# Kernel optimization log

Hardware: AMD Instinct MI355X
Metric: run time of the kernel (lower is better)

The kernel has to match this reference:

```python
import jax, jax.numpy as jnp
import numpy as np

F = 256

def setup_inputs() -> dict:
    key = jax.random.key(0)
    ks = jax.random.split(key, 6)
    s = 1.0 / np.sqrt(F)
    x = jax.random.normal(ks[0], (16, 1024, F), dtype=jnp.float32)
    W_alpha = jax.random.uniform(ks[1], (F, F), minval=-s, maxval=s, dtype=jnp.float32)
    W_beta = jax.random.uniform(ks[2], (F, F), minval=-s, maxval=s, dtype=jnp.float32)
    W_unary = jax.random.uniform(ks[3], (F, F), minval=-s, maxval=s, dtype=jnp.float32)
    b_unary = jax.random.uniform(ks[4], (F,), minval=-s, maxval=s, dtype=jnp.float32)
    W_r = jax.random.uniform(ks[5], (F, F), minval=-s, maxval=s, dtype=jnp.float32)
    return {"x": x, "W_alpha": W_alpha, "W_beta": W_beta, "W_unary": W_unary, "b_unary": b_unary, "W_r": W_r}

def reference(x, W_alpha, W_beta, W_unary, b_unary, W_r):
    # x: [B, N, F]; torch Linear computes x @ W^T (+ b)
    B, N, _ = x.shape
    alpha = jnp.einsum('bnf,gf->bng', x, W_alpha)
    beta = jnp.einsum('bnf,gf->bng', x, W_beta)
    unary = jnp.einsum('bnf,gf->bng', x, W_unary) + b_unary
    # scores: alpha_i . beta_j, diagonal excluded (i == j skipped in loop)
    scores = jnp.einsum('bif,bjf->bij', alpha, beta)
    scores = scores * (1.0 - jnp.eye(N, dtype=x.dtype))
    att = jnp.einsum('bij,bjf->bif', scores, unary) / N
    out = jnp.einsum('bif,gf->big', att, W_r) + x
    return out
```

## Files before the change

kernel.cpp:

```cpp
#include <hip/hip_runtime.h>


typedef __bf16 bf16;
typedef float floatx4 __attribute__((ext_vector_type(4)));
typedef bf16 bf16x8 __attribute__((ext_vector_type(8)));
typedef bf16 bf16x4 __attribute__((ext_vector_type(4)));

constexpr int FD = 256;
constexpr int NB = 16;
constexpr int NN = 1024;
constexpr int RR = NB * NN;

__device__ __forceinline__ bf16x8 cvt8(float4 a, float4 b) {
    bf16x8 o = { (bf16)a.x, (bf16)a.y, (bf16)a.z, (bf16)a.w,
                 (bf16)b.x, (bf16)b.y, (bf16)b.z, (bf16)b.w };
    return o;
}

__global__ __launch_bounds__(256)
void prep(const float* __restrict__ Wu, const float* __restrict__ bu, const float* __restrict__ Wr,
          bf16* __restrict__ Wcb, float* __restrict__ bc)
{
    const int blk = blockIdx.x, tid = threadIdx.x;
    if (blk < 256) {
        const int j = blk;
        float acc = 0.0f;
        for (int g = 0; g < FD; g += 4) {
            float4 wr = *(const float4*)&Wr[j * FD + g];
            acc += wr.x * Wu[g * FD + tid] + wr.y * Wu[(g + 1) * FD + tid]
                 + wr.z * Wu[(g + 2) * FD + tid] + wr.w * Wu[(g + 3) * FD + tid];
        }
        Wcb[j * FD + tid] = (bf16)acc;
    } else {
        float s = 0.0f;
        for (int g = 0; g < FD; g++) s += Wr[tid * FD + g] * bu[g];
        bc[tid] = s;
    }
}

__global__ __launch_bounds__(256)
void proj3(const float* __restrict__ x,
           const float* __restrict__ Wa, const float* __restrict__ Wb, const bf16* __restrict__ Wc,
           bf16* __restrict__ alpha, bf16* __restrict__ U2,
           bf16* __restrict__ betaT, bf16* __restrict__ U2T,
           const float* __restrict__ bc, float* __restrict__ dpart)
{
    constexpr int BM = 128, BN = 64, BK = 32, LDK = 36;
    __shared__ bf16 As[BM][LDK];
    __shared__ bf16 Bs[3][BN][LDK];
    __shared__ bf16 Tr[8960];
    const int tid = threadIdx.x;
    const int wave = tid >> 6, lane = tid & 63;
    const int q = lane >> 4, l16 = lane & 15;
    const int bm = blockIdx.y * BM, bn = blockIdx.x * BN;

    const int rowA0 = tid >> 2,          k8A0 = (tid & 3) * 8;
    const int rowA1 = (tid + 256) >> 2,  k8A1 = (tid & 3) * 8;
    const int rowW  = tid >> 2,          k8W  = (tid & 3) * 8;

    bf16x8 pxa0, pxa1, pwa, pwb; int4 pwc;
#define PROJ_LOAD(KK) do { \
        const float* s0 = &x[(size_t)(bm + rowA0) * FD + (KK) + k8A0]; \
        pxa0 = cvt8(*(const float4*)s0, *(const float4*)(s0 + 4)); \
        const float* s1 = &x[(size_t)(bm + rowA1) * FD + (KK) + k8A1]; \
        pxa1 = cvt8(*(const float4*)s1, *(const float4*)(s1 + 4)); \
        const float* sa = &Wa[(size_t)(bn + rowW) * FD + (KK) + k8W]; \
        pwa = cvt8(*(const float4*)sa, *(const float4*)(sa + 4)); \
        const float* sb = &Wb[(size_t)(bn + rowW) * FD + (KK) + k8W]; \
        pwb = cvt8(*(const float4*)sb, *(const float4*)(sb + 4)); \
        pwc = *(const int4*)&Wc[(size_t)(bn + rowW) * FD + (KK) + k8W]; \
    } while (0)

    floatx4 acc[3][2][4] = {};
    PROJ_LOAD(0);

    for (int k0 = 0; k0 < FD; k0 += BK) {
        *(bf16x8*)&As[rowA0][k8A0] = pxa0;
        *(bf16x8*)&As[rowA1][k8A1] = pxa1;
        *(bf16x8*)&Bs[0][rowW][k8W] = pwa;
        *(bf16x8*)&Bs[1][rowW][k8W] = pwb;
        *(int4*)&Bs[2][rowW][k8W] = pwc;
        __syncthreads();
        if (k0 + BK < FD) PROJ_LOAD(k0 + BK);
        bf16x8 af[2];
        #pragma unroll
        for (int mi = 0; mi < 2; mi++)
            af[mi] = *(const bf16x8*)&As[wave * 32 + mi * 16 + l16][q * 8];
        #pragma unroll
        for (int w = 0; w < 3; w++) {
            bf16x8 bq[4];
            #pragma unroll
            for (int nj = 0; nj < 4; nj++)
                bq[nj] = *(const bf16x8*)&Bs[w][nj * 16 + l16][q * 8];
            #pragma unroll
            for (int mi = 0; mi < 2; mi++)
                #pragma unroll
                for (int nj = 0; nj < 4; nj++)
                    acc[w][mi][nj] = __builtin_amdgcn_mfma_f32_16x16x32_bf16(af[mi], bq[nj], acc[w][mi][nj], 0, 0, 0);
        }
        __syncthreads();
    }
#undef PROJ_LOAD

    const int b = bm >> 10, n0 = bm & (NN - 1);
    float bcv[4];
    #pragma unroll
    for (int nj = 0; nj < 4; nj++) bcv[nj] = bc[bn + nj * 16 + l16];

    #pragma unroll
    for (int mi = 0; mi < 2; mi++)
        #pragma unroll
        for (int i = 0; i < 4; i++) {
            float p = 0.0f;
            #pragma unroll
            for (int nj = 0; nj < 4; nj++)
                p += acc[0][mi][nj][i] * acc[1][mi][nj][i];
            #pragma unroll
            for (int off = 1; off < 16; off <<= 1) p += __shfl_xor(p, off);
            if (l16 == 0) {
                int m = bm + wave * 32 + mi * 16 + q * 4 + i;
                dpart[(size_t)blockIdx.x * RR + m] = p;
            }
        }

    #pragma unroll
    for (int pass = 0; pass < 2; pass++) {
        const int w = pass ? 2 : 0;
        __syncthreads();
        #pragma unroll
        for (int mi = 0; mi < 2; mi++)
            #pragma unroll
            for (int i = 0; i < 4; i++) {
                int ml = wave * 32 + mi * 16 + q * 4 + i;
                #pragma unroll
                for (int nj = 0; nj < 4; nj++) {
                    float v = acc[w][mi][nj][i];
                    if (w == 2) v += bcv[nj];
                    Tr[ml * 68 + nj * 16 + l16] = (bf16)v;
                }
            }
        __syncthreads();
        bf16* dst = pass ? U2 : alpha;
        #pragma unroll
        for (int it = 0; it < 4; it++) {
            int c = tid + it * 256;
            int row = c >> 3, chunk = c & 7;
            bf16x8 v = *(const bf16x8*)&Tr[row * 68 + chunk * 8];
            *(bf16x8*)&dst[(size_t)(bm + row) * FD + bn + chunk * 8] = v;
        }
    }

    #pragma unroll
    for (int pass = 0; pass < 2; pass++) {
        const int w = pass ? 2 : 1;
        __syncthreads();
        #pragma unroll
        for (int mi = 0; mi < 2; mi++)
            #pragma unroll
            for (int nj = 0; nj < 4; nj++) {
                bf16x4 v4;
                #pragma unroll
                for (int i = 0; i < 4; i++) {
                    float v = acc[w][mi][nj][i];
                    if (w == 2) v += bcv[nj];
                    v4[i] = (bf16)v;
                }
                *(bf16x4*)&Tr[(nj * 16 + l16) * 140 + wave * 32 + mi * 16 + q * 4] = v4;
            }
        __syncthreads();
        bf16* dst = (pass ? U2T : betaT) + (size_t)b * FD * NN;
        #pragma unroll
        for (int it = 0; it < 4; it++) {
            int c = tid + it * 256;
            int row = c >> 4, chunk = c & 15;
            bf16x8 v = *(const bf16x8*)&Tr[row * 140 + chunk * 8];
            *(bf16x8*)&dst[(size_t)(bn + row) * NN + n0 + chunk * 8] = v;
        }
    }
}

__global__ __launch_bounds__(256)
void m2_mfma(const bf16* __restrict__ U2T, const bf16* __restrict__ betaT, bf16* __restrict__ M2t)
{
    constexpr int LDK = 36;
    __shared__ bf16 As[64][LDK];
    __shared__ bf16 Bs[64][LDK];
    __shared__ bf16 Tr[64 * 68];
    const int tid = threadIdx.x;
    const int wave = tid >> 6, lane = tid & 63;
    const int q = lane >> 4, l16 = lane & 15;
    const int wj = wave >> 1, wk = wave & 1;
    const int b = blockIdx.z;
    const int bj = blockIdx.y * 64, bk = blockIdx.x * 64;
    const int row = tid >> 2, k8 = (tid & 3) * 8;
    const bf16* Arow = U2T + (size_t)b * FD * NN + (size_t)(bj + row) * NN + k8;
    const bf16* Brow = betaT + (size_t)b * FD * NN + (size_t)(bk + row) * NN + k8;

    int4 ra = *(const int4*)&Arow[0];
    int4 rb = *(const int4*)&Brow[0];
    floatx4 acc[2][2] = {};
    for (int n0 = 0; n0 < NN; n0 += 32) {
        *(int4*)&As[row][k8] = ra;
        *(int4*)&Bs[row][k8] = rb;
        __syncthreads();
        if (n0 + 32 < NN) { ra = *(const int4*)&Arow[n0 + 32]; rb = *(const int4*)&Brow[n0 + 32]; }
        bf16x8 af[2], bq[2];
        #pragma unroll
        for (int mi = 0; mi < 2; mi++)
            af[mi] = *(const bf16x8*)&As[wj * 32 + mi * 16 + l16][q * 8];
        #pragma unroll
        for (int kj = 0; kj < 2; kj++)
            bq[kj] = *(const bf16x8*)&Bs[wk * 32 + kj * 16 + l16][q * 8];
        #pragma unroll
        for (int mi = 0; mi < 2; mi++)
            #pragma unroll
            for (int kj = 0; kj < 2; kj++)
                acc[mi][kj] = __builtin_amdgcn_mfma_f32_16x16x32_bf16(af[mi], bq[kj], acc[mi][kj], 0, 0, 0);
        __syncthreads();
    }
    __syncthreads();
    #pragma unroll
    for (int mi = 0; mi < 2; mi++)
        #pragma unroll
        for (int i = 0; i < 4; i++) {
            int jl = wj * 32 + mi * 16 + q * 4 + i;
            #pragma unroll
            for (int kj = 0; kj < 2; kj++)
                Tr[jl * 68 + wk * 32 + kj * 16 + l16] = (bf16)acc[mi][kj][i];
        }
    __syncthreads();
    bf16* Mb = M2t + (size_t)b * FD * FD;
    #pragma unroll
    for (int it = 0; it < 2; it++) {
        int c = tid + it * 256;
        int r = c >> 3, chunk = c & 7;
        bf16x8 v = *(const bf16x8*)&Tr[r * 68 + chunk * 8];
        *(bf16x8*)&Mb[(size_t)(bj + r) * FD + bk + chunk * 8] = v;
    }
}

__global__ __launch_bounds__(256)
void final_mfma(const bf16* __restrict__ alpha, const bf16* __restrict__ M2t,
                const float* __restrict__ dpart, const bf16* __restrict__ U2,
                const float* __restrict__ x, float* __restrict__ out)
{
    constexpr int BM = 128, BN = 64, BK = 32, LDK = 36;
    __shared__ bf16 As[BM][LDK];
    __shared__ bf16 Bs[BN][LDK];
    const int tid = threadIdx.x;
    const int wave = tid >> 6, lane = tid & 63;
    const int q = lane >> 4, l16 = lane & 15;
    const int bm = blockIdx.y * BM, bn = blockIdx.x * BN;
    const bf16* Qb = M2t + (size_t)(bm >> 10) * FD * FD;

    const int rowA0 = tid >> 2,         k8A0 = (tid & 3) * 8;
    const int rowA1 = (tid + 256) >> 2, k8A1 = (tid & 3) * 8;
    const int rowB  = tid >> 2,         k8B  = (tid & 3) * 8;

    int4 ra0 = *(const int4*)&alpha[(size_t)(bm + rowA0) * FD + k8A0];
    int4 ra1 = *(const int4*)&alpha[(size_t)(bm + rowA1) * FD + k8A1];
    int4 rb  = *(const int4*)&Qb[(size_t)(bn + rowB) * FD + k8B];

    floatx4 acc[2][4] = {};
    for (int k0 = 0; k0 < FD; k0 += BK) {
        *(int4*)&As[rowA0][k8A0] = ra0;
        *(int4*)&As[rowA1][k8A1] = ra1;
        *(int4*)&Bs[rowB][k8B] = rb;
        __syncthreads();
        if (k0 + BK < FD) {
            ra0 = *(const int4*)&alpha[(size_t)(bm + rowA0) * FD + k0 + BK + k8A0];
            ra1 = *(const int4*)&alpha[(size_t)(bm + rowA1) * FD + k0 + BK + k8A1];
            rb  = *(const int4*)&Qb[(size_t)(bn + rowB) * FD + k0 + BK + k8B];
        }
        bf16x8 af[2], bq[4];
        #pragma unroll
        for (int mi = 0; mi < 2; mi++)
            af[mi] = *(const bf16x8*)&As[wave * 32 + mi * 16 + l16][q * 8];
        #pragma unroll
        for (int nj = 0; nj < 4; nj++)
            bq[nj] = *(const bf16x8*)&Bs[nj * 16 + l16][q * 8];
        #pragma unroll
        for (int mi = 0; mi < 2; mi++)
            #pragma unroll
            for (int nj = 0; nj < 4; nj++)
                acc[mi][nj] = __builtin_amdgcn_mfma_f32_16x16x32_bf16(af[mi], bq[nj], acc[mi][nj], 0, 0, 0);
        __syncthreads();
    }

    #pragma unroll
    for (int mi = 0; mi < 2; mi++)
        #pragma unroll
        for (int i = 0; i < 4; i++) {
            int m = bm + wave * 32 + mi * 16 + q * 4 + i;
            float d = dpart[m] + dpart[RR + m] + dpart[2 * RR + m] + dpart[3 * RR + m];
            #pragma unroll
            for (int nj = 0; nj < 4; nj++) {
                int n = bn + nj * 16 + l16;
                float v = (acc[mi][nj][i] - d * (float)U2[(size_t)m * FD + n]) * (1.0f / 1024.0f);
                out[(size_t)m * FD + n] = v + x[(size_t)m * FD + n];
            }
        }
}

extern "C" void kernel_launch(void* const* d_in, const int* in_sizes, int n_in,
                              void* d_out, int out_size, void* d_ws, size_t ws_size,
                              hipStream_t stream)
{
    const float* x  = (const float*)d_in[0];
    const float* Wa = (const float*)d_in[1];
    const float* Wb = (const float*)d_in[2];
    const float* Wu = (const float*)d_in[3];
    const float* bu = (const float*)d_in[4];
    const float* Wr = (const float*)d_in[5];
    float* out = (float*)d_out;

    char* w = (char*)d_ws;
    bf16* Wcb   = (bf16*)w;  w += (size_t)FD * FD * 2;
    float* bc   = (float*)w; w += (size_t)FD * 4;
    bf16* alpha = (bf16*)w;  w += (size_t)RR * FD * 2;
    bf16* U2    = (bf16*)w;  w += (size_t)RR * FD * 2;
    bf16* betaT = (bf16*)w;  w += (size_t)RR * FD * 2;
    bf16* U2T   = (bf16*)w;  w += (size_t)RR * FD * 2;
    bf16* M2t   = (bf16*)w;  w += (size_t)NB * FD * FD * 2;
    float* dpart= (float*)w; w += (size_t)4 * RR * 4;

    dim3 blk(256);

    prep<<<dim3(257), blk, 0, stream>>>(Wu, bu, Wr, Wcb, bc);

    proj3<<<dim3(FD / 64, RR / 128), blk, 0, stream>>>(x, Wa, Wb, Wcb,
                                                       alpha, U2, betaT, U2T, bc, dpart);

    m2_mfma<<<dim3(FD / 64, FD / 64, NB), blk, 0, stream>>>(U2T, betaT, M2t);

    final_mfma<<<dim3(FD / 64, RR / 128), blk, 0, stream>>>(alpha, M2t, dpart, U2, x, out);
}
```

Baseline: 127.8 us.

## Split-K the M2 reduction, shrink proj/final tiles to 64x64 with BK=64

The M2 GEMM over the sequence dimension is split into four chunks across more blocks, writing fp32 partials that a new reduction kernel sums and converts to bf16. The proj3 and final kernels move from 128-row to 64-row tiles with a K-step of 64 and a wider LDS row stride, which doubles their grid size. The goal is more parallelism and occupancy, since m2 previously launched only 256 blocks. The cost is an extra kernel launch, fp32 partial traffic, and more redundant weight loads per row tile.

```diff
diff --git a/kernel.cpp b/kernel.cpp
--- a/kernel.cpp
+++ b/kernel.cpp
@@ -45,58 +45,64 @@
            bf16* __restrict__ betaT, bf16* __restrict__ U2T,
            const float* __restrict__ bc, float* __restrict__ dpart)
 {
-    constexpr int BM = 128, BN = 64, BK = 32, LDK = 36;
-    __shared__ bf16 As[BM][LDK];
-    __shared__ bf16 Bs[3][BN][LDK];
-    __shared__ bf16 Tr[8960];
+    constexpr int LDK = 68, WSZ = 64 * LDK;
+    __shared__ __align__(16) bf16 smem[4 * WSZ];
+    bf16* As = smem;
+    bf16* Bs = smem + WSZ;
+    bf16* Tr = smem;
     const int tid = threadIdx.x;
     const int wave = tid >> 6, lane = tid & 63;
     const int q = lane >> 4, l16 = lane & 15;
-    const int bm = blockIdx.y * BM, bn = blockIdx.x * BN;
-
-    const int rowA0 = tid >> 2,          k8A0 = (tid & 3) * 8;
-    const int rowA1 = (tid + 256) >> 2,  k8A1 = (tid & 3) * 8;
-    const int rowW  = tid >> 2,          k8W  = (tid & 3) * 8;
-
-    bf16x8 pxa0, pxa1, pwa, pwb; int4 pwc;
+    const int bm = blockIdx.y * 64, bn = blockIdx.x * 64;
+
+    const int row0 = tid >> 3, k8 = (tid & 7) * 8;
+
+    bf16x8 pA[2], pW0[2], pW1[2]; int4 pW2[2];
 #define PROJ_LOAD(KK) do { \
-        const float* s0 = &x[(size_t)(bm + rowA0) * FD + (KK) + k8A0]; \
-        pxa0 = cvt8(*(const float4*)s0, *(const float4*)(s0 + 4)); \
-        const float* s1 = &x[(size_t)(bm + rowA1) * FD + (KK) + k8A1]; \
-        pxa1 = cvt8(*(const float4*)s1, *(const float4*)(s1 + 4)); \
-        const float* sa = &Wa[(size_t)(bn + rowW) * FD + (KK) + k8W]; \
-        pwa = cvt8(*(const float4*)sa, *(const float4*)(sa + 4)); \
-        const float* sb = &Wb[(size_t)(bn + rowW) * FD + (KK) + k8W]; \
-        pwb = cvt8(*(const float4*)sb, *(const float4*)(sb + 4)); \
-        pwc = *(const int4*)&Wc[(size_t)(bn + rowW) * FD + (KK) + k8W]; \
+        const float* s0 = &x[(size_t)(bm + row0) * FD + (KK) + k8]; \
+        pA[0] = cvt8(*(const float4*)s0, *(const float4*)(s0 + 4)); \
+        const float* s1 = &x[(size_t)(bm + row0 + 32) * FD + (KK) + k8]; \
+        pA[1] = cvt8(*(const float4*)s1, *(const float4*)(s1 + 4)); \
+        const float* a0 = &Wa[(size_t)(bn + row0) * FD + (KK) + k8]; \
+        pW0[0] = cvt8(*(const float4*)a0, *(const float4*)(a0 + 4)); \
+        const float* a1 = &Wa[(size_t)(bn + row0 + 32) * FD + (KK) + k8]; \
+        pW0[1] = cvt8(*(const float4*)a1, *(const float4*)(a1 + 4)); \
+        const float* b0 = &Wb[(size_t)(bn + row0) * FD + (KK) + k8]; \
+        pW1[0] = cvt8(*(const float4*)b0, *(const float4*)(b0 + 4)); \
+        const float* b1 = &Wb[(size_t)(bn + row0 + 32) * FD + (KK) + k8]; \
+        pW1[1] = cvt8(*(const float4*)b1, *(const float4*)(b1 + 4)); \
+        pW2[0] = *(const int4*)&Wc[(size_t)(bn + row0) * FD + (KK) + k8]; \
+        pW2[1] = *(const int4*)&Wc[(size_t)(bn + row0 + 32) * FD + (KK) + k8]; \
     } while (0)
 
-    floatx4 acc[3][2][4] = {};
+    floatx4 acc[3][4] = {};
     PROJ_LOAD(0);
 
-    for (int k0 = 0; k0 < FD; k0 += BK) {
-        *(bf16x8*)&As[rowA0][k8A0] = pxa0;
-        *(bf16x8*)&As[rowA1][k8A1] = pxa1;
-        *(bf16x8*)&Bs[0][rowW][k8W] = pwa;
-        *(bf16x8*)&Bs[1][rowW][k8W] = pwb;
-        *(int4*)&Bs[2][rowW][k8W] = pwc;
-        __syncthreads();
-        if (k0 + BK < FD) PROJ_LOAD(k0 + BK);
+    for (int k0 = 0; k0 < FD; k0 += 64) {
+        *(bf16x8*)&As[row0 * LDK + k8] = pA[0];
+        *(bf16x8*)&As[(row0 + 32) * LDK + k8] = pA[1];
+        *(bf16x8*)&Bs[0 * WSZ + row0 * LDK + k8] = pW0[0];
+        *(bf16x8*)&Bs[0 * WSZ + (row0 + 32) * LDK + k8] = pW0[1];
+        *(bf16x8*)&Bs[1 * WSZ + row0 * LDK + k8] = pW1[0];
+        *(bf16x8*)&Bs[1 * WSZ + (row0 + 32) * LDK + k8] = pW1[1];
+        *(int4*)&Bs[2 * WSZ + row0 * LDK + k8] = pW2[0];
+        *(int4*)&Bs[2 * WSZ + (row0 + 32) * LDK + k8] = pW2[1];
+        __syncthreads();
+        if (k0 + 64 < FD) PROJ_LOAD(k0 + 64);
         bf16x8 af[2];
         #pragma unroll
-        for (int mi = 0; mi < 2; mi++)
-            af[mi] = *(const bf16x8*)&As[wave * 32 + mi * 16 + l16][q * 8];
+        for (int h = 0; h < 2; h++)
+            af[h] = *(const bf16x8*)&As[(wave * 16 + l16) * LDK + h * 32 + q * 8];
         #pragma unroll
         for (int w = 0; w < 3; w++) {
-            bf16x8 bq[4];
-            #pragma unroll
-            for (int nj = 0; nj < 4; nj++)
-                bq[nj] = *(const bf16x8*)&Bs[w][nj * 16 + l16][q * 8];
-            #pragma unroll
-            for (int mi = 0; mi < 2; mi++)
+            #pragma unroll
+            for (int h = 0; h < 2; h++) {
                 #pragma unroll
-                for (int nj = 0; nj < 4; nj++)
-                    acc[w][mi][nj] = __builtin_amdgcn_mfma_f32_16x16x32_bf16(af[mi], bq[nj], acc[w][mi][nj], 0, 0, 0);
+                for (int nj = 0; nj < 4; nj++) {
+                    bf16x8 bq = *(const bf16x8*)&Bs[w * WSZ + (nj * 16 + l16) * LDK + h * 32 + q * 8];
+                    acc[w][nj] = __builtin_amdgcn_mfma_f32_16x16x32_bf16(af[h], bq, acc[w][nj], 0, 0, 0);
+                }
+            }
         }
         __syncthreads();
     }
@@ -108,41 +114,37 @@
     for (int nj = 0; nj < 4; nj++) bcv[nj] = bc[bn + nj * 16 + l16];
 
     #pragma unroll
-    for (int mi = 0; mi < 2; mi++)
-        #pragma unroll
-        for (int i = 0; i < 4; i++) {
-            float p = 0.0f;
-            #pragma unroll
-            for (int nj = 0; nj < 4; nj++)
-                p += acc[0][mi][nj][i] * acc[1][mi][nj][i];
-            #pragma unroll
-            for (int off = 1; off < 16; off <<= 1) p += __shfl_xor(p, off);
-            if (l16 == 0) {
-                int m = bm + wave * 32 + mi * 16 + q * 4 + i;
-                dpart[(size_t)blockIdx.x * RR + m] = p;
-            }
-        }
+    for (int i = 0; i < 4; i++) {
+        float p = 0.0f;
+        #pragma unroll
+        for (int nj = 0; nj < 4; nj++)
+            p += acc[0][nj][i] * acc[1][nj][i];
+        #pragma unroll
+        for (int off = 1; off < 16; off <<= 1) p += __shfl_xor(p, off);
+        if (l16 == 0) {
+            int m = bm + wave * 16 + q * 4 + i;
+            dpart[(size_t)blockIdx.x * RR + m] = p;
+        }
+    }
 
     #pragma unroll
     for (int pass = 0; pass < 2; pass++) {
         const int w = pass ? 2 : 0;
         __syncthreads();
         #pragma unroll
-        for (int mi = 0; mi < 2; mi++)
-            #pragma unroll
-            for (int i = 0; i < 4; i++) {
-                int ml = wave * 32 + mi * 16 + q * 4 + i;
-                #pragma unroll
-                for (int nj = 0; nj < 4; nj++) {
-                    float v = acc[w][mi][nj][i];
-                    if (w == 2) v += bcv[nj];
-                    Tr[ml * 68 + nj * 16 + l16] = (bf16)v;
-                }
+        for (int i = 0; i < 4; i++) {
+            int ml = wave * 16 + q * 4 + i;
+            #pragma unroll
+            for (int nj = 0; nj < 4; nj++) {
+                float v = acc[w][nj][i];
+                if (w == 2) v += bcv[nj];
+                Tr[ml * 68 + nj * 16 + l16] = (bf16)v;
             }
+        }
         __syncthreads();
         bf16* dst = pass ? U2 : alpha;
         #pragma unroll
-        for (int it = 0; it < 4; it++) {
+        for (int it = 0; it < 2; it++) {
             int c = tid + it * 256;
             int row = c >> 3, chunk = c & 7;
             bf16x8 v = *(const bf16x8*)&Tr[row * 68 + chunk * 8];
@@ -155,88 +157,109 @@
         const int w = pass ? 2 : 1;
         __syncthreads();
         #pragma unroll
-        for (int mi = 0; mi < 2; mi++)
-            #pragma unroll
-            for (int nj = 0; nj < 4; nj++) {
-                bf16x4 v4;
-                #pragma unroll
-                for (int i = 0; i < 4; i++) {
-                    float v = acc[w][mi][nj][i];
-                    if (w == 2) v += bcv[nj];
-                    v4[i] = (bf16)v;
-                }
-                *(bf16x4*)&Tr[(nj * 16 + l16) * 140 + wave * 32 + mi * 16 + q * 4] = v4;
+        for (int nj = 0; nj < 4; nj++) {
+            bf16x4 v4;
+            #pragma unroll
+            for (int i = 0; i < 4; i++) {
+                float v = acc[w][nj][i];
+                if (w == 2) v += bcv[nj];
+                v4[i] = (bf16)v;
             }
+            *(bf16x4*)&Tr[(nj * 16 + l16) * 72 + wave * 16 + q * 4] = v4;
+        }
         __syncthreads();
         bf16* dst = (pass ? U2T : betaT) + (size_t)b * FD * NN;
         #pragma unroll
-        for (int it = 0; it < 4; it++) {
+        for (int it = 0; it < 2; it++) {
             int c = tid + it * 256;
-            int row = c >> 4, chunk = c & 15;
-            bf16x8 v = *(const bf16x8*)&Tr[row * 140 + chunk * 8];
+            int row = c >> 3, chunk = c & 7;
+            bf16x8 v = *(const bf16x8*)&Tr[row * 72 + chunk * 8];
             *(bf16x8*)&dst[(size_t)(bn + row) * NN + n0 + chunk * 8] = v;
         }
     }
 }
 
 __global__ __launch_bounds__(256)
-void m2_mfma(const bf16* __restrict__ U2T, const bf16* __restrict__ betaT, bf16* __restrict__ M2t)
-{
-    constexpr int LDK = 36;
-    __shared__ bf16 As[64][LDK];
-    __shared__ bf16 Bs[64][LDK];
-    __shared__ bf16 Tr[64 * 68];
+void m2_mfma(const bf16* __restrict__ U2T, const bf16* __restrict__ betaT, float* __restrict__ Mpart)
+{
+    constexpr int LDK = 68;
+    __shared__ __align__(16) bf16 As[64 * LDK];
+    __shared__ __align__(16) bf16 Bs[64 * LDK];
     const int tid = threadIdx.x;
     const int wave = tid >> 6, lane = tid & 63;
     const int q = lane >> 4, l16 = lane & 15;
     const int wj = wave >> 1, wk = wave & 1;
-    const int b = blockIdx.z;
+    const int b = blockIdx.z >> 2, ch = blockIdx.z & 3;
     const int bj = blockIdx.y * 64, bk = blockIdx.x * 64;
-    const int row = tid >> 2, k8 = (tid & 3) * 8;
-    const bf16* Arow = U2T + (size_t)b * FD * NN + (size_t)(bj + row) * NN + k8;
-    const bf16* Brow = betaT + (size_t)b * FD * NN + (size_t)(bk + row) * NN + k8;
-
-    int4 ra = *(const int4*)&Arow[0];
-    int4 rb = *(const int4*)&Brow[0];
+    const int nb = ch * 256;
+    const int row0 = tid >> 3, k8 = (tid & 7) * 8;
+    const bf16* Ap = U2T + (size_t)b * FD * NN;
+    const bf16* Bp = betaT + (size_t)b * FD * NN;
+
+    int4 ra[2], rb[2];
+    ra[0] = *(const int4*)&Ap[(size_t)(bj + row0) * NN + nb + k8];
+    ra[1] = *(const int4*)&Ap[(size_t)(bj + row0 + 32) * NN + nb + k8];
+    rb[0] = *(const int4*)&Bp[(size_t)(bk + row0) * NN + nb + k8];
+    rb[1] = *(const int4*)&Bp[(size_t)(bk + row0 + 32) * NN + nb + k8];
+
     floatx4 acc[2][2] = {};
-    for (int n0 = 0; n0 < NN; n0 += 32) {
-        *(int4*)&As[row][k8] = ra;
-        *(int4*)&Bs[row][k8] = rb;
-        __syncthreads();
-        if (n0 + 32 < NN) { ra = *(const int4*)&Arow[n0 + 32]; rb = *(const int4*)&Brow[n0 + 32]; }
-        bf16x8 af[2], bq[2];
-        #pragma unroll
-        for (int mi = 0; mi < 2; mi++)
-            af[mi] = *(const bf16x8*)&As[wj * 32 + mi * 16 + l16][q * 8];
-        #pragma unroll
-        for (int kj = 0; kj < 2; kj++)
-            bq[kj] = *(const bf16x8*)&Bs[wk * 32 + kj * 16 + l16][q * 8];
-        #pragma unroll
-        for (int mi = 0; mi < 2; mi++)
+    for (int nc = 0; nc < 256; nc += 64) {
+        *(int4*)&As[row0 * LDK + k8] = ra[0];
+        *(int4*)&As[(row0 + 32) * LDK + k8] = ra[1];
+        *(int4*)&Bs[row0 * LDK + k8] = rb[0];
+        *(int4*)&Bs[(row0 + 32) * LDK + k8] = rb[1];
+        __syncthreads();
+        if (nc + 64 < 256) {
+            int nn = nb + nc + 64;
+            ra[0] = *(const int4*)&Ap[(size_t)(bj + row0) * NN + nn + k8];
+            ra[1] = *(const int4*)&Ap[(size_t)(bj + row0 + 32) * NN + nn + k8];
+            rb[0] = *(const int4*)&Bp[(size_t)(bk + row0) * NN + nn + k8];
+            rb[1] = *(const int4*)&Bp[(size_t)(bk + row0 + 32) * NN + nn + k8];
+        }
+        #pragma unroll
+        for (int h = 0; h < 2; h++) {
+            bf16x8 af[2], bq[2];
+            #pragma unroll
+            for (int mi = 0; mi < 2; mi++)
+                af[mi] = *(const bf16x8*)&As[(wj * 32 + mi * 16 + l16) * LDK + h * 32 + q * 8];
             #pragma unroll
             for (int kj = 0; kj < 2; kj++)
-                acc[mi][kj] = __builtin_amdgcn_mfma_f32_16x16x32_bf16(af[mi], bq[kj], acc[mi][kj], 0, 0, 0);
-        __syncthreads();
-    }
-    __syncthreads();
+                bq[kj] = *(const bf16x8*)&Bs[(wk * 32 + kj * 16 + l16) * LDK + h * 32 + q * 8];
+            #pragma unroll
+            for (int mi = 0; mi < 2; mi++)
+                #pragma unroll
+                for (int kj = 0; kj < 2; kj++)
+                    acc[mi][kj] = __builtin_amdgcn_mfma_f32_16x16x32_bf16(af[mi], bq[kj], acc[mi][kj], 0, 0, 0);
+        }
+        __syncthreads();
+    }
+
+    float* P = Mpart + ((size_t)ch * NB + b) * FD * FD;
     #pragma unroll
     for (int mi = 0; mi < 2; mi++)
         #pragma unroll
         for (int i = 0; i < 4; i++) {
-            int jl = wj * 32 + mi * 16 + q * 4 + i;
+            int j = bj + wj * 32 + mi * 16 + q * 4 + i;
             #pragma unroll
             for (int kj = 0; kj < 2; kj++)
-                Tr[jl * 68 + wk * 32 + kj * 16 + l16] = (bf16)acc[mi][kj][i];
-        }
-    __syncthreads();
-    bf16* Mb = M2t + (size_t)b * FD * FD;
-    #pragma unroll
-    for (int it = 0; it < 2; it++) {
-        int c = tid + it * 256;
-        int r = c >> 3, chunk = c & 7;
-        bf16x8 v = *(const bf16x8*)&Tr[r * 68 + chunk * 8];
-        *(bf16x8*)&Mb[(size_t)(bj + r) * FD + bk + chunk * 8] = v;
-    }
+                P[(size_t)j * FD + bk + wk * 32 + kj * 16 + l16] = acc[mi][kj][i];
+        }
+}
+
+__global__ __launch_bounds__(256)
+void mred(const float* __restrict__ Mpart, bf16* __restrict__ M2t)
+{
+    const size_t S = (size_t)NB * FD * FD;
+    size_t i = ((size_t)blockIdx.x * 256 + threadIdx.x) * 8;
+    float4 a0 = *(const float4*)&Mpart[i],         a1 = *(const float4*)&Mpart[i + 4];
+    float4 b0 = *(const float4*)&Mpart[S + i],     b1 = *(const float4*)&Mpart[S + i + 4];
+    float4 c0 = *(const float4*)&Mpart[2*S + i],   c1 = *(const float4*)&Mpart[2*S + i + 4];
+    float4 d0 = *(const float4*)&Mpart[3*S + i],   d1 = *(const float4*)&Mpart[3*S + i + 4];
+    bf16x8 o = { (bf16)(a0.x + b0.x + c0.x + d0.x), (bf16)(a0.y + b0.y + c0.y + d0.y),
+                 (bf16)(a0.z + b0.z + c0.z + d0.z), (bf16)(a0.w + b0.w + c0.w + d0.w),
+                 (bf16)(a1.x + b1.x + c1.x + d1.x), (bf16)(a1.y + b1.y + c1.y + d1.y),
+                 (bf16)(a1.z + b1.z + c1.z + d1.z), (bf16)(a1.w + b1.w + c1.w + d1.w) };
+    *(bf16x8*)&M2t[i] = o;
 }
 
 __global__ __launch_bounds__(256)
@@ -244,62 +267,58 @@
                 const float* __restrict__ dpart, const bf16* __restrict__ U2,
                 const float* __restrict__ x, float* __restrict__ out)
 {
-    constexpr int BM = 128, BN = 64, BK = 32, LDK = 36;
-    __shared__ bf16 As[BM][LDK];
-    __shared__ bf16 Bs[BN][LDK];
+    constexpr int LDK = 68;
+    __shared__ __align__(16) bf16 As[64 * LDK];
+    __shared__ __align__(16) bf16 Bs[64 * LDK];
     const int tid = threadIdx.x;
     const int wave = tid >> 6, lane = tid & 63;
     const int q = lane >> 4, l16 = lane & 15;
-    const int bm = blockIdx.y * BM, bn = blockIdx.x * BN;
+    const int bm = blockIdx.y * 64, bn = blockIdx.x * 64;
     const bf16* Qb = M2t + (size_t)(bm >> 10) * FD * FD;
-
-    const int rowA0 = tid >> 2,         k8A0 = (tid & 3) * 8;
-    const int rowA1 = (tid + 256) >> 2, k8A1 = (tid & 3) * 8;
-    const int rowB  = tid >> 2,         k8B  = (tid & 3) * 8;
-
-    int4 ra0 = *(const int4*)&alpha[(size_t)(bm + rowA0) * FD + k8A0];
-    int4 ra1 = *(const int4*)&alpha[(size_t)(bm + rowA1) * FD + k8A1];
-    int4 rb  = *(const int4*)&Qb[(size_t)(bn + rowB) * FD + k8B];
-
-    floatx4 acc[2][4] = {};
-    for (int k0 = 0; k0 < FD; k0 += BK) {
-        *(int4*)&As[rowA0][k8A0] = ra0;
-        *(int4*)&As[rowA1][k8A1] = ra1;
-        *(int4*)&Bs[rowB][k8B] = rb;
-        __syncthreads();
-        if (k0 + BK < FD) {
-            ra0 = *(const int4*)&alpha[(size_t)(bm + rowA0) * FD + k0 + BK + k8A0];
-            ra1 = *(const int4*)&alpha[(size_t)(bm + rowA1) * FD + k0 + BK + k8A1];
-            rb  = *(const int4*)&Qb[(size_t)(bn + rowB) * FD + k0 + BK + k8B];
-        }
-        bf16x8 af[2], bq[4];
-        #pragma unroll
-        for (int mi = 0; mi < 2; mi++)
-            af[mi] = *(const bf16x8*)&As[wave * 32 + mi * 16 + l16][q * 8];
-        #pragma unroll
-        for (int nj = 0; nj < 4; nj++)
-            bq[nj] = *(const bf16x8*)&Bs[nj * 16 + l16][q * 8];
-        #pragma unroll
-        for (int mi = 0; mi < 2; mi++)
-            #pragma unroll
-            for (int nj = 0; nj < 4; nj++)
-                acc[mi][nj] = __builtin_amdgcn_mfma_f32_16x16x32_bf16(af[mi], bq[nj], acc[mi][nj], 0, 0, 0);
-        __syncthreads();
-    }
-
-    #pragma unroll
-    for (int mi = 0; mi < 2; mi++)
-        #pragma unroll
-        for (int i = 0; i < 4; i++) {
-            int m = bm + wave * 32 + mi * 16 + q * 4 + i;
-            float d = dpart[m] + dpart[RR + m] + dpart[2 * RR + m] + dpart[3 * RR + m];
+    const int row0 = tid >> 3, k8 = (tid & 7) * 8;
+
+    int4 ra[2], rb[2];
+    ra[0] = *(const int4*)&alpha[(size_t)(bm + row0) * FD + k8];
+    ra[1] = *(const int4*)&alpha[(size_t)(bm + row0 + 32) * FD + k8];
+    rb[0] = *(const int4*)&Qb[(size_t)(bn + row0) * FD + k8];
+    rb[1] = *(const int4*)&Qb[(size_t)(bn + row0 + 32) * FD + k8];
+
+    floatx4 acc[4] = {};
+    for (int k0 = 0; k0 < FD; k0 += 64) {
+        *(int4*)&As[row0 * LDK + k8] = ra[0];
+        *(int4*)&As[(row0 + 32) * LDK + k8] = ra[1];
+        *(int4*)&Bs[row0 * LDK + k8] = rb[0];
+        *(int4*)&Bs[(row0 + 32) * LDK + k8] = rb[1];
+        __syncthreads();
+        if (k0 + 64 < FD) {
+            ra[0] = *(const int4*)&alpha[(size_t)(bm + row0) * FD + k0 + 64 + k8];
+            ra[1] = *(const int4*)&alpha[(size_t)(bm + row0 + 32) * FD + k0 + 64 + k8];
+            rb[0] = *(const int4*)&Qb[(size_t)(bn + row0) * FD + k0 + 64 + k8];
+            rb[1] = *(const int4*)&Qb[(size_t)(bn + row0 + 32) * FD + k0 + 64 + k8];
+        }
+        #pragma unroll
+        for (int h = 0; h < 2; h++) {
+            bf16x8 af = *(const bf16x8*)&As[(wave * 16 + l16) * LDK + h * 32 + q * 8];
             #pragma unroll
             for (int nj = 0; nj < 4; nj++) {
-                int n = bn + nj * 16 + l16;
-                float v = (acc[mi][nj][i] - d * (float)U2[(size_t)m * FD + n]) * (1.0f / 1024.0f);
-                out[(size_t)m * FD + n] = v + x[(size_t)m * FD + n];
+                bf16x8 bq = *(const bf16x8*)&Bs[(nj * 16 + l16) * LDK + h * 32 + q * 8];
+                acc[nj] = __builtin_amdgcn_mfma_f32_16x16x32_bf16(af, bq, acc[nj], 0, 0, 0);
             }
         }
+        __syncthreads();
+    }
+
+    #pragma unroll
+    for (int i = 0; i < 4; i++) {
+        int m = bm + wave * 16 + q * 4 + i;
+        float d = dpart[m] + dpart[RR + m] + dpart[2 * RR + m] + dpart[3 * RR + m];
+        #pragma unroll
+        for (int nj = 0; nj < 4; nj++) {
+            int n = bn + nj * 16 + l16;
+            float v = (acc[nj][i] - d * (float)U2[(size_t)m * FD + n]) * (1.0f / 1024.0f);
+            out[(size_t)m * FD + n] = v + x[(size_t)m * FD + n];
+        }
+    }
 }
 
 extern "C" void kernel_launch(void* const* d_in, const int* in_sizes, int n_in,
@@ -323,15 +342,18 @@
     bf16* U2T   = (bf16*)w;  w += (size_t)RR * FD * 2;
     bf16* M2t   = (bf16*)w;  w += (size_t)NB * FD * FD * 2;
     float* dpart= (float*)w; w += (size_t)4 * RR * 4;
+    float* Mpart= (float*)w; w += (size_t)4 * NB * FD * FD * 4;
 
     dim3 blk(256);
 
     prep<<<dim3(257), blk, 0, stream>>>(Wu, bu, Wr, Wcb, bc);
 
-    proj3<<<dim3(FD / 64, RR / 128), blk, 0, stream>>>(x, Wa, Wb, Wcb,
-                                                       alpha, U2, betaT, U2T, bc, dpart);
-
-    m2_mfma<<<dim3(FD / 64, FD / 64, NB), blk, 0, stream>>>(U2T, betaT, M2t);
-
-    final_mfma<<<dim3(FD / 64, RR / 128), blk, 0, stream>>>(alpha, M2t, dpart, U2, x, out);
-}
+    proj3<<<dim3(FD / 64, RR / 64), blk, 0, stream>>>(x, Wa, Wb, Wcb,
+                                                      alpha, U2, betaT, U2T, bc, dpart);
+
+    m2_mfma<<<dim3(FD / 64, FD / 64, NB * 4), blk, 0, stream>>>(U2T, betaT, Mpart);
+
+    mred<<<dim3(512), blk, 0, stream>>>(Mpart, M2t);
+
+    final_mfma<<<dim3(FD / 64, RR / 64), blk, 0, stream>>>(alpha, M2t, dpart, U2, x, out);
+}
```

After: 202.0 us. +58.0%, slower.

## Fuse all stages into one cooperative persistent kernel with grid syncs

Applied to the files above, without the earlier changes.

Merges the prep, projection, M2 and final GEMM kernels into a single cooperative launch of 512 blocks that separates stages with grid.sync. Prep now also converts Wa and Wb to bf16 so the projection loads bf16 weights directly. The M2 stage uses a 64-wide K step to halve the number of loop iterations. The aim is to remove launch gaps and per-block conversion work. In exchange there are grid-wide barriers, a fixed grid size that limits parallelism in each stage, and a fallback to separate kernels if the cooperative launch fails.

```diff
diff --git a/kernel.cpp b/kernel.cpp
--- a/kernel.cpp
+++ b/kernel.cpp
@@ -1,4 +1,7 @@
 #include <hip/hip_runtime.h>
+#include <hip/hip_cooperative_groups.h>
+
+namespace cg = cooperative_groups;
 
 
 typedef __bf16 bf16;
@@ -17,81 +20,91 @@
     return o;
 }
 
-__global__ __launch_bounds__(256)
-void prep(const float* __restrict__ Wu, const float* __restrict__ bu, const float* __restrict__ Wr,
-          bf16* __restrict__ Wcb, float* __restrict__ bc)
-{
-    const int blk = blockIdx.x, tid = threadIdx.x;
-    if (blk < 256) {
-        const int j = blk;
-        float acc = 0.0f;
-        for (int g = 0; g < FD; g += 4) {
-            float4 wr = *(const float4*)&Wr[j * FD + g];
-            acc += wr.x * Wu[g * FD + tid] + wr.y * Wu[(g + 1) * FD + tid]
-                 + wr.z * Wu[(g + 2) * FD + tid] + wr.w * Wu[(g + 3) * FD + tid];
-        }
-        Wcb[j * FD + tid] = (bf16)acc;
-    } else {
+__device__ __forceinline__ void dev_prep(int blk, int tid,
+    const float* __restrict__ Wa, const float* __restrict__ Wb,
+    const float* __restrict__ Wu, const float* __restrict__ bu, const float* __restrict__ Wr,
+    bf16* __restrict__ Wab, bf16* __restrict__ Wbb, bf16* __restrict__ Wcb, float* __restrict__ bc)
+{
+    if (blk < 16) {
+        int w = blk >> 3, wb = blk & 7;
+        const float* src = (w == 0) ? Wa : Wb;
+        bf16* dst = (w == 0) ? Wab : Wbb;
+        for (int it = 0; it < 8; it++) {
+            int i = wb * 8192 + it * 1024 + tid * 4;
+            float4 v = *(const float4*)&src[i];
+            bf16x4 o = { (bf16)v.x, (bf16)v.y, (bf16)v.z, (bf16)v.w };
+            *(bf16x4*)&dst[i] = o;
+        }
+    } else if (blk < 80) {
+        int j0 = (blk - 16) * 4;
+        float acc[4] = {};
+        for (int g = 0; g < FD; g++) {
+            float wu = Wu[g * FD + tid];
+            #pragma unroll
+            for (int jr = 0; jr < 4; jr++)
+                acc[jr] += Wr[(j0 + jr) * FD + g] * wu;
+        }
+        #pragma unroll
+        for (int jr = 0; jr < 4; jr++)
+            Wcb[(j0 + jr) * FD + tid] = (bf16)acc[jr];
+    } else if (blk == 80) {
         float s = 0.0f;
         for (int g = 0; g < FD; g++) s += Wr[tid * FD + g] * bu[g];
         bc[tid] = s;
     }
 }
 
-__global__ __launch_bounds__(256)
-void proj3(const float* __restrict__ x,
-           const float* __restrict__ Wa, const float* __restrict__ Wb, const bf16* __restrict__ Wc,
-           bf16* __restrict__ alpha, bf16* __restrict__ U2,
-           bf16* __restrict__ betaT, bf16* __restrict__ U2T,
-           const float* __restrict__ bc, float* __restrict__ dpart)
-{
-    constexpr int BM = 128, BN = 64, BK = 32, LDK = 36;
-    __shared__ bf16 As[BM][LDK];
-    __shared__ bf16 Bs[3][BN][LDK];
-    __shared__ bf16 Tr[8960];
-    const int tid = threadIdx.x;
+__device__ __forceinline__ void dev_proj(int bx, int by, int tid, char* smemraw,
+    const float* __restrict__ x,
+    const bf16* __restrict__ Wab, const bf16* __restrict__ Wbb, const bf16* __restrict__ Wcb,
+    const float* __restrict__ bc,
+    bf16* __restrict__ alpha, bf16* __restrict__ U2,
+    bf16* __restrict__ betaT, bf16* __restrict__ U2T, float* __restrict__ dpart)
+{
+    constexpr int LDK = 36;
+    bf16* As = (bf16*)smemraw;
+    bf16* Bs = (bf16*)(smemraw + 9216);
+    bf16* Tr = (bf16*)(smemraw + 23040);
     const int wave = tid >> 6, lane = tid & 63;
     const int q = lane >> 4, l16 = lane & 15;
-    const int bm = blockIdx.y * BM, bn = blockIdx.x * BN;
-
-    const int rowA0 = tid >> 2,          k8A0 = (tid & 3) * 8;
-    const int rowA1 = (tid + 256) >> 2,  k8A1 = (tid & 3) * 8;
-    const int rowW  = tid >> 2,          k8W  = (tid & 3) * 8;
-
-    bf16x8 pxa0, pxa1, pwa, pwb; int4 pwc;
-#define PROJ_LOAD(KK) do { \
-        const float* s0 = &x[(size_t)(bm + rowA0) * FD + (KK) + k8A0]; \
+    const int bm = by * 128, bn = bx * 64;
+
+    const int rowA0 = tid >> 2, k8A = (tid & 3) * 8;
+    const int rowA1 = rowA0 + 64;
+    const int rowW = tid >> 2, k8W = (tid & 3) * 8;
+
+    bf16x8 pxa0, pxa1; int4 pwa, pwb, pwc;
+#define PLOAD(KK) do { \
+        const float* s0 = &x[(size_t)(bm + rowA0) * FD + (KK) + k8A]; \
         pxa0 = cvt8(*(const float4*)s0, *(const float4*)(s0 + 4)); \
-        const float* s1 = &x[(size_t)(bm + rowA1) * FD + (KK) + k8A1]; \
+        const float* s1 = &x[(size_t)(bm + rowA1) * FD + (KK) + k8A]; \
         pxa1 = cvt8(*(const float4*)s1, *(const float4*)(s1 + 4)); \
-        const float* sa = &Wa[(size_t)(bn + rowW) * FD + (KK) + k8W]; \
-        pwa = cvt8(*(const float4*)sa, *(const float4*)(sa + 4)); \
-        const float* sb = &Wb[(size_t)(bn + rowW) * FD + (KK) + k8W]; \
-        pwb = cvt8(*(const float4*)sb, *(const float4*)(sb + 4)); \
-        pwc = *(const int4*)&Wc[(size_t)(bn + rowW) * FD + (KK) + k8W]; \
+        pwa = *(const int4*)&Wab[(size_t)(bn + rowW) * FD + (KK) + k8W]; \
+        pwb = *(const int4*)&Wbb[(size_t)(bn + rowW) * FD + (KK) + k8W]; \
+        pwc = *(const int4*)&Wcb[(size_t)(bn + rowW) * FD + (KK) + k8W]; \
     } while (0)
 
     floatx4 acc[3][2][4] = {};
-    PROJ_LOAD(0);
-
-    for (int k0 = 0; k0 < FD; k0 += BK) {
-        *(bf16x8*)&As[rowA0][k8A0] = pxa0;
-        *(bf16x8*)&As[rowA1][k8A1] = pxa1;
-        *(bf16x8*)&Bs[0][rowW][k8W] = pwa;
-        *(bf16x8*)&Bs[1][rowW][k8W] = pwb;
-        *(int4*)&Bs[2][rowW][k8W] = pwc;
-        __syncthreads();
-        if (k0 + BK < FD) PROJ_LOAD(k0 + BK);
+    PLOAD(0);
+
+    for (int k0 = 0; k0 < FD; k0 += 32) {
+        *(bf16x8*)&As[rowA0 * LDK + k8A] = pxa0;
+        *(bf16x8*)&As[rowA1 * LDK + k8A] = pxa1;
+        *(int4*)&Bs[(0 * 64 + rowW) * LDK + k8W] = pwa;
+        *(int4*)&Bs[(1 * 64 + rowW) * LDK + k8W] = pwb;
+        *(int4*)&Bs[(2 * 64 + rowW) * LDK + k8W] = pwc;
+        __syncthreads();
+        if (k0 + 32 < FD) PLOAD(k0 + 32);
         bf16x8 af[2];
         #pragma unroll
         for (int mi = 0; mi < 2; mi++)
-            af[mi] = *(const bf16x8*)&As[wave * 32 + mi * 16 + l16][q * 8];
+            af[mi] = *(const bf16x8*)&As[(wave * 32 + mi * 16 + l16) * LDK + q * 8];
         #pragma unroll
         for (int w = 0; w < 3; w++) {
             bf16x8 bq[4];
             #pragma unroll
             for (int nj = 0; nj < 4; nj++)
-                bq[nj] = *(const bf16x8*)&Bs[w][nj * 16 + l16][q * 8];
+                bq[nj] = *(const bf16x8*)&Bs[(w * 64 + nj * 16 + l16) * LDK + q * 8];
             #pragma unroll
             for (int mi = 0; mi < 2; mi++)
                 #pragma unroll
@@ -100,7 +113,7 @@
         }
         __syncthreads();
     }
-#undef PROJ_LOAD
+#undef PLOAD
 
     const int b = bm >> 10, n0 = bm & (NN - 1);
     float bcv[4];
@@ -119,7 +132,7 @@
             for (int off = 1; off < 16; off <<= 1) p += __shfl_xor(p, off);
             if (l16 == 0) {
                 int m = bm + wave * 32 + mi * 16 + q * 4 + i;
-                dpart[(size_t)blockIdx.x * RR + m] = p;
+                dpart[(size_t)bx * RR + m] = p;
             }
         }
 
@@ -179,43 +192,56 @@
     }
 }
 
-__global__ __launch_bounds__(256)
-void m2_mfma(const bf16* __restrict__ U2T, const bf16* __restrict__ betaT, bf16* __restrict__ M2t)
-{
-    constexpr int LDK = 36;
-    __shared__ bf16 As[64][LDK];
-    __shared__ bf16 Bs[64][LDK];
-    __shared__ bf16 Tr[64 * 68];
-    const int tid = threadIdx.x;
+__device__ __forceinline__ void dev_m2(int blk, int tid, char* smemraw,
+    const bf16* __restrict__ U2T, const bf16* __restrict__ betaT, bf16* __restrict__ M2t)
+{
+    constexpr int LDK = 68;
+    bf16* As = (bf16*)smemraw;
+    bf16* Bs = (bf16*)(smemraw + 8704);
+    bf16* Tr = (bf16*)(smemraw + 17408);
     const int wave = tid >> 6, lane = tid & 63;
     const int q = lane >> 4, l16 = lane & 15;
     const int wj = wave >> 1, wk = wave & 1;
-    const int b = blockIdx.z;
-    const int bj = blockIdx.y * 64, bk = blockIdx.x * 64;
-    const int row = tid >> 2, k8 = (tid & 3) * 8;
-    const bf16* Arow = U2T + (size_t)b * FD * NN + (size_t)(bj + row) * NN + k8;
-    const bf16* Brow = betaT + (size_t)b * FD * NN + (size_t)(bk + row) * NN + k8;
-
-    int4 ra = *(const int4*)&Arow[0];
-    int4 rb = *(const int4*)&Brow[0];
+    const int b = blk >> 4, rem = blk & 15;
+    const int bj = (rem >> 2) * 64, bk = (rem & 3) * 64;
+    const int row0 = tid >> 3, k8 = (tid & 7) * 8;
+    const bf16* Ap = U2T + (size_t)b * FD * NN;
+    const bf16* Bp = betaT + (size_t)b * FD * NN;
+
+    int4 ra[2], rb[2];
+    ra[0] = *(const int4*)&Ap[(size_t)(bj + row0) * NN + k8];
+    ra[1] = *(const int4*)&Ap[(size_t)(bj + row0 + 32) * NN + k8];
+    rb[0] = *(const int4*)&Bp[(size_t)(bk + row0) * NN + k8];
+    rb[1] = *(const int4*)&Bp[(size_t)(bk + row0 + 32) * NN + k8];
+
     floatx4 acc[2][2] = {};
-    for (int n0 = 0; n0 < NN; n0 += 32) {
-        *(int4*)&As[row][k8] = ra;
-        *(int4*)&Bs[row][k8] = rb;
-        __syncthreads();
-        if (n0 + 32 < NN) { ra = *(const int4*)&Arow[n0 + 32]; rb = *(const int4*)&Brow[n0 + 32]; }
-        bf16x8 af[2], bq[2];
-        #pragma unroll
-        for (int mi = 0; mi < 2; mi++)
-            af[mi] = *(const bf16x8*)&As[wj * 32 + mi * 16 + l16][q * 8];
-        #pragma unroll
-        for (int kj = 0; kj < 2; kj++)
-            bq[kj] = *(const bf16x8*)&Bs[wk * 32 + kj * 16 + l16][q * 8];
-        #pragma unroll
-        for (int mi = 0; mi < 2; mi++)
+    for (int n0 = 0; n0 < NN; n0 += 64) {
+        *(int4*)&As[row0 * LDK + k8] = ra[0];
+        *(int4*)&As[(row0 + 32) * LDK + k8] = ra[1];
+        *(int4*)&Bs[row0 * LDK + k8] = rb[0];
+        *(int4*)&Bs[(row0 + 32) * LDK + k8] = rb[1];
+        __syncthreads();
+        if (n0 + 64 < NN) {
+            ra[0] = *(const int4*)&Ap[(size_t)(bj + row0) * NN + n0 + 64 + k8];
+            ra[1] = *(const int4*)&Ap[(size_t)(bj + row0 + 32) * NN + n0 + 64 + k8];
+            rb[0] = *(const int4*)&Bp[(size_t)(bk + row0) * NN + n0 + 64 + k8];
+            rb[1] = *(const int4*)&Bp[(size_t)(bk + row0 + 32) * NN + n0 + 64 + k8];
+        }
+        #pragma unroll
+        for (int h = 0; h < 2; h++) {
+            bf16x8 af[2], bq[2];
+            #pragma unroll
+            for (int mi = 0; mi < 2; mi++)
+                af[mi] = *(const bf16x8*)&As[(wj * 32 + mi * 16 + l16) * LDK + h * 32 + q * 8];
             #pragma unroll
             for (int kj = 0; kj < 2; kj++)
-                acc[mi][kj] = __builtin_amdgcn_mfma_f32_16x16x32_bf16(af[mi], bq[kj], acc[mi][kj], 0, 0, 0);
+                bq[kj] = *(const bf16x8*)&Bs[(wk * 32 + kj * 16 + l16) * LDK + h * 32 + q * 8];
+            #pragma unroll
+            for (int mi = 0; mi < 2; mi++)
+                #pragma unroll
+                for (int kj = 0; kj < 2; kj++)
+                    acc[mi][kj] = __builtin_amdgcn_mfma_f32_16x16x32_bf16(af[mi], bq[kj], acc[mi][kj], 0, 0, 0);
+        }
         __syncthreads();
     }
     __syncthreads();
@@ -239,46 +265,45 @@
     }
 }
 
-__global__ __launch_bounds__(256)
-void final_mfma(const bf16* __restrict__ alpha, const bf16* __restrict__ M2t,
-                const float* __restrict__ dpart, const bf16* __restrict__ U2,
-                const float* __restrict__ x, float* __restrict__ out)
-{
-    constexpr int BM = 128, BN = 64, BK = 32, LDK = 36;
-    __shared__ bf16 As[BM][LDK];
-    __shared__ bf16 Bs[BN][LDK];
-    const int tid = threadIdx.x;
+__device__ __forceinline__ void dev_final(int bx, int by, int tid, char* smemraw,
+    const bf16* __restrict__ alpha, const bf16* __restrict__ M2t,
+    const float* __restrict__ dpart, const bf16* __restrict__ U2,
+    const float* __restrict__ x, float* __restrict__ out)
+{
+    constexpr int LDK = 36;
+    bf16* As = (bf16*)smemraw;
+    bf16* Bs = (bf16*)(smemraw + 9216);
     const int wave = tid >> 6, lane = tid & 63;
     const int q = lane >> 4, l16 = lane & 15;
-    const int bm = blockIdx.y * BM, bn = blockIdx.x * BN;
+    const int bm = by * 128, bn = bx * 64;
     const bf16* Qb = M2t + (size_t)(bm >> 10) * FD * FD;
 
-    const int rowA0 = tid >> 2,         k8A0 = (tid & 3) * 8;
-    const int rowA1 = (tid + 256) >> 2, k8A1 = (tid & 3) * 8;
-    const int rowB  = tid >> 2,         k8B  = (tid & 3) * 8;
-
-    int4 ra0 = *(const int4*)&alpha[(size_t)(bm + rowA0) * FD + k8A0];
-    int4 ra1 = *(const int4*)&alpha[(size_t)(bm + rowA1) * FD + k8A1];
+    const int rowA0 = tid >> 2, k8A = (tid & 3) * 8;
+    const int rowA1 = rowA0 + 64;
+    const int rowB = tid >> 2, k8B = (tid & 3) * 8;
+
+    int4 ra0 = *(const int4*)&alpha[(size_t)(bm + rowA0) * FD + k8A];
+    int4 ra1 = *(const int4*)&alpha[(size_t)(bm + rowA1) * FD + k8A];
     int4 rb  = *(const int4*)&Qb[(size_t)(bn + rowB) * FD + k8B];
 
     floatx4 acc[2][4] = {};
-    for (int k0 = 0; k0 < FD; k0 += BK) {
-        *(int4*)&As[rowA0][k8A0] = ra0;
-        *(int4*)&As[rowA1][k8A1] = ra1;
-        *(int4*)&Bs[rowB][k8B] = rb;
-        __syncthreads();
-        if (k0 + BK < FD) {
-            ra0 = *(const int4*)&alpha[(size_t)(bm + rowA0) * FD + k0 + BK + k8A0];
-            ra1 = *(const int4*)&alpha[(size_t)(bm + rowA1) * FD + k0 + BK + k8A1];
-            rb  = *(const int4*)&Qb[(size_t)(bn + rowB) * FD + k0 + BK + k8B];
+    for (int k0 = 0; k0 < FD; k0 += 32) {
+        *(int4*)&As[rowA0 * LDK + k8A] = ra0;
+        *(int4*)&As[rowA1 * LDK + k8A] = ra1;
+        *(int4*)&Bs[rowB * LDK + k8B] = rb;
+        __syncthreads();
+        if (k0 + 32 < FD) {
+            ra0 = *(const int4*)&alpha[(size_t)(bm + rowA0) * FD + k0 + 32 + k8A];
+            ra1 = *(const int4*)&alpha[(size_t)(bm + rowA1) * FD + k0 + 32 + k8A];
+            rb  = *(const int4*)&Qb[(size_t)(bn + rowB) * FD + k0 + 32 + k8B];
         }
         bf16x8 af[2], bq[4];
         #pragma unroll
         for (int mi = 0; mi < 2; mi++)
-            af[mi] = *(const bf16x8*)&As[wave * 32 + mi * 16 + l16][q * 8];
+            af[mi] = *(const bf16x8*)&As[(wave * 32 + mi * 16 + l16) * LDK + q * 8];
         #pragma unroll
         for (int nj = 0; nj < 4; nj++)
-            bq[nj] = *(const bf16x8*)&Bs[nj * 16 + l16][q * 8];
+            bq[nj] = *(const bf16x8*)&Bs[(nj * 16 + l16) * LDK + q * 8];
         #pragma unroll
         for (int mi = 0; mi < 2; mi++)
             #pragma unroll
@@ -300,6 +325,62 @@
                 out[(size_t)m * FD + n] = v + x[(size_t)m * FD + n];
             }
         }
+}
+
+__global__ __launch_bounds__(256, 2)
+void fused(const float* x, const float* Wa, const float* Wb, const float* Wu,
+           const float* bu, const float* Wr,
+           bf16* Wab, bf16* Wbb, bf16* Wcb, float* bc,
+           bf16* alpha, bf16* U2, bf16* betaT, bf16* U2T, bf16* M2t,
+           float* dpart, float* out)
+{
+    __shared__ __align__(16) char smem[40960];
+    cg::grid_group grid = cg::this_grid();
+    const int blk = blockIdx.x, tid = threadIdx.x;
+
+    dev_prep(blk, tid, Wa, Wb, Wu, bu, Wr, Wab, Wbb, Wcb, bc);
+    __threadfence();
+    grid.sync();
+
+    dev_proj(blk & 3, blk >> 2, tid, smem, x, Wab, Wbb, Wcb, bc, alpha, U2, betaT, U2T, dpart);
+    __threadfence();
+    grid.sync();
+
+    if (blk < 256) dev_m2(blk, tid, smem, U2T, betaT, M2t);
+    __threadfence();
+    grid.sync();
+
+    dev_final(blk & 3, blk >> 2, tid, smem, alpha, M2t, dpart, U2, x, out);
+}
+
+__global__ __launch_bounds__(256)
+void prep_k(const float* Wa, const float* Wb, const float* Wu, const float* bu, const float* Wr,
+            bf16* Wab, bf16* Wbb, bf16* Wcb, float* bc)
+{
+    dev_prep(blockIdx.x, threadIdx.x, Wa, Wb, Wu, bu, Wr, Wab, Wbb, Wcb, bc);
+}
+
+__global__ __launch_bounds__(256)
+void proj_k(const float* x, const bf16* Wab, const bf16* Wbb, const bf16* Wcb, const float* bc,
+            bf16* alpha, bf16* U2, bf16* betaT, bf16* U2T, float* dpart)
+{
+    __shared__ __align__(16) char smem[40960];
+    dev_proj(blockIdx.x, blockIdx.y, threadIdx.x, smem, x, Wab, Wbb, Wcb, bc, alpha, U2, betaT, U2T, dpart);
+}
+
+__global__ __launch_bounds__(256)
+void m2_k(const bf16* U2T, const bf16* betaT, bf16* M2t)
+{
+    __shared__ __align__(16) char smem[26112];
+    dev_m2(blockIdx.x, threadIdx.x, smem, U2T, betaT, M2t);
+}
+
+__global__ __launch_bounds__(256)
+void final_k(const bf16* alpha, const bf16* M2t, const float* dpart, const bf16* U2,
+             const float* x, float* out)
+{
+    __shared__ __align__(16) char smem[13824];
+    dev_final(blockIdx.x, blockIdx.y, threadIdx.x, smem, alpha, M2t, dpart, U2, x, out);
 }
 
 extern "C" void kernel_launch(void* const* d_in, const int* in_sizes, int n_in,
@@ -315,6 +396,8 @@
     float* out = (float*)d_out;
 
     char* w = (char*)d_ws;
+    bf16* Wab   = (bf16*)w;  w += (size_t)FD * FD * 2;
+    bf16* Wbb   = (bf16*)w;  w += (size_t)FD * FD * 2;
     bf16* Wcb   = (bf16*)w;  w += (size_t)FD * FD * 2;
     float* bc   = (float*)w; w += (size_t)FD * 4;
     bf16* alpha = (bf16*)w;  w += (size_t)RR * FD * 2;
@@ -324,14 +407,18 @@
     bf16* M2t   = (bf16*)w;  w += (size_t)NB * FD * FD * 2;
     float* dpart= (float*)w; w += (size_t)4 * RR * 4;
 
-    dim3 blk(256);
-
-    prep<<<dim3(257), blk, 0, stream>>>(Wu, bu, Wr, Wcb, bc);
-
-    proj3<<<dim3(FD / 64, RR / 128), blk, 0, stream>>>(x, Wa, Wb, Wcb,
-                                                       alpha, U2, betaT, U2T, bc, dpart);
-
-    m2_mfma<<<dim3(FD / 64, FD / 64, NB), blk, 0, stream>>>(U2T, betaT, M2t);
-
-    final_mfma<<<dim3(FD / 64, RR / 128), blk, 0, stream>>>(alpha, M2t, dpart, U2, x, out);
-}
+    void* args[] = { (void*)&x, (void*)&Wa, (void*)&Wb, (void*)&Wu, (void*)&bu, (void*)&Wr,
+                     (void*)&Wab, (void*)&Wbb, (void*)&Wcb, (void*)&bc,
+                     (void*)&alpha, (void*)&U2, (void*)&betaT, (void*)&U2T, (void*)&M2t,
+                     (void*)&dpart, (void*)&out };
+
+    hipError_t err = hipLaunchCooperativeKernel((const void*)fused, dim3(512), dim3(256),
+                                                args, 0, stream);
+    if (err != hipSuccess) {
+        prep_k<<<dim3(81), dim3(256), 0, stream>>>(Wa, Wb, Wu, bu, Wr, Wab, Wbb, Wcb, bc);
+        proj_k<<<dim3(4, 128), dim3(256), 0, stream>>>(x, Wab, Wbb, Wcb, bc,
+                                                       alpha, U2, betaT, U2T, dpart);
+        m2_k<<<dim3(256), dim3(256), 0, stream>>>(U2T, betaT, M2t);
+        final_k<<<dim3(4, 128), dim3(256), 0, stream>>>(alpha, M2t, dpart, U2, x, out);
+    }
+}
```

New measurement: 507.0 us. 297% more time.
